# Kernel tuning notes

Hardware: AMD Instinct MI355X
Metric: run time of the kernel (lower is better)

The kernel has to match this reference:

```python
import jax, jax.numpy as jnp
import numpy as np

WINDOW_SIZE = 5  # hardcoded in module __init__


def local_window_mask(T, dtype=jnp.float32):
    # Faithful to torch code: start from triu(ones, diagonal=1) (value 1.0 for
    # j > i, NOT -inf!), then set entries outside the band |j - i| <= sz to -inf.
    sz = WINDOW_SIZE // 2
    i = jnp.arange(T)[:, None]
    j = jnp.arange(T)[None, :]
    upper = (j > i).astype(dtype)            # triu part contributes +1 bias
    in_band = jnp.abs(j - i) <= sz
    return jnp.where(in_band, upper, jnp.float32(-jnp.inf).astype(dtype))


def setup_inputs() -> dict:
    key = jax.random.key(0)
    kx, kq, kk, kv = jax.random.split(key, 4)
    B, T, C = 4, 4096, 64
    head_size = 64
    s = 1.0 / np.sqrt(C)
    return {
        "x": jax.random.normal(kx, (B, T, C), dtype=jnp.float32),
        "Wq": jax.random.normal(kq, (head_size, C), dtype=jnp.float32) * s,
        "Wk": jax.random.normal(kk, (head_size, C), dtype=jnp.float32) * s,
        "Wv": jax.random.normal(kv, (head_size, C), dtype=jnp.float32) * s,
    }


def reference(x, Wq, Wk, Wv):
    B, T, C = x.shape
    # nn.Linear(d_model, head_size, bias=False): y = x @ W.T
    q = jnp.einsum('btc,hc->bth', x, Wq)
    k = jnp.einsum('btc,hc->bth', x, Wk)
    v = jnp.einsum('btc,hc->bth', x, Wv)
    scale = jnp.asarray(C, x.dtype) ** -0.5   # scale uses input dim C
    scores = jnp.einsum('bth,bsh->bts', q, k) * scale + local_window_mask(T, x.dtype)
    attn = jax.nn.softmax(scores, axis=-1)    # original computes this twice; once suffices (same math)
    op = jnp.einsum('bts,bsh->bth', attn, v)
    return (op, attn)
```

## Files before the change

kernel.cpp:

```cpp
#include <hip/hip_runtime.h>

constexpr int B      = 4;
constexpr int T      = 4096;
constexpr int C      = 64;
constexpr int H      = 64;
constexpr int TILE   = 32;
constexpr int HALO   = 2;
constexpr int HR     = TILE + 2 * HALO;
constexpr int LS     = 68;
constexpr int NT     = 256;
constexpr int NTILES = T / TILE;

__device__ __forceinline__ void compute_mat(float (*__restrict__ dst)[LS],
                                            const float (*__restrict__ sXl)[LS],
                                            const float (*__restrict__ sWl)[LS],
                                            const int rows, const int srcOff,
                                            const int tid)
{
    const int nrt = rows >> 2;
    if (tid < nrt * 8) {
        const int rt = tid >> 3;
        const int h0 = (tid & 7) << 3;
        int r[4];
#pragma unroll
        for (int k = 0; k < 4; ++k) r[k] = rt + k * nrt + srcOff;

        float acc[4][8];
#pragma unroll
        for (int k = 0; k < 4; ++k)
#pragma unroll
            for (int j = 0; j < 8; ++j) acc[k][j] = 0.f;

        for (int c4 = 0; c4 < C; c4 += 4) {
            float xv[4][4];
#pragma unroll
            for (int k = 0; k < 4; ++k)
                *(float4*)&xv[k][0] = *(const float4*)&sXl[r[k]][c4];
#pragma unroll
            for (int cc = 0; cc < 4; ++cc) {
                const float4 wA = *(const float4*)&sWl[c4 + cc][h0];
                const float4 wB = *(const float4*)&sWl[c4 + cc][h0 + 4];
#pragma unroll
                for (int k = 0; k < 4; ++k) {
                    const float xs = xv[k][cc];
                    acc[k][0] = fmaf(xs, wA.x, acc[k][0]);
                    acc[k][1] = fmaf(xs, wA.y, acc[k][1]);
                    acc[k][2] = fmaf(xs, wA.z, acc[k][2]);
                    acc[k][3] = fmaf(xs, wA.w, acc[k][3]);
                    acc[k][4] = fmaf(xs, wB.x, acc[k][4]);
                    acc[k][5] = fmaf(xs, wB.y, acc[k][5]);
                    acc[k][6] = fmaf(xs, wB.z, acc[k][6]);
                    acc[k][7] = fmaf(xs, wB.w, acc[k][7]);
                }
            }
        }
#pragma unroll
        for (int k = 0; k < 4; ++k) {
            const int rr = r[k] - srcOff;
            *(float4*)&dst[rr][h0]     = make_float4(acc[k][0], acc[k][1], acc[k][2], acc[k][3]);
            *(float4*)&dst[rr][h0 + 4] = make_float4(acc[k][4], acc[k][5], acc[k][6], acc[k][7]);
        }
    }
}

__global__ __launch_bounds__(NT, 2)
void sparse_attn_fused(const float* __restrict__ x,
                       const float* __restrict__ Wq,
                       const float* __restrict__ Wk,
                       const float* __restrict__ Wv,
                       float* __restrict__ out)
{
    __shared__ float sX[HR][LS];
    __shared__ float sW[C][LS];
    __shared__ float sQ[TILE][LS];
    __shared__ float sK[HR][LS];
    __shared__ float sV[HR][LS];
    __shared__ float sS[TILE][8];

    const int tid  = threadIdx.x;
    const int b    = blockIdx.x / NTILES;
    const int tile = blockIdx.x % NTILES;
    const int row0 = tile * TILE;
    const float* xb = x + (size_t)b * T * C;
    const size_t attnBase = (size_t)B * T * H;
    float* attnBlock = out + attnBase + ((size_t)b * T + row0) * T;

    for (int s = tid; s < HR * (C / 4); s += NT) {
        const int lr = s >> 4;
        const int c4 = (s & 15) << 2;
        const int gr = row0 + lr - HALO;
        float4 v = make_float4(0.f, 0.f, 0.f, 0.f);
        if (gr >= 0 && gr < T) v = *(const float4*)(xb + (size_t)gr * C + c4);
        *(float4*)&sX[lr][c4] = v;
    }
    for (int s = tid; s < C * H; s += NT) sW[s & 63][s >> 6] = Wq[s];
    {
        float4* dst = (float4*)attnBlock;
        const float4 z = make_float4(0.f, 0.f, 0.f, 0.f);
        for (int s = tid; s < TILE * (T / 4); s += NT) dst[s] = z;
    }
    __syncthreads();

    compute_mat(sQ, sX, sW, TILE, HALO, tid);
    __syncthreads();

    for (int s = tid; s < C * H; s += NT) sW[s & 63][s >> 6] = Wk[s];
    __syncthreads();

    compute_mat(sK, sX, sW, HR, 0, tid);
    __syncthreads();

    if (tid < TILE * 5) {
        const int i  = tid / 5;
        const int dj = tid % 5;
        const int jg = row0 + i - HALO + dj;
        float sc = -__builtin_inff();
        if (jg >= 0 && jg < T) {
            float acc = 0.f;
#pragma unroll
            for (int h4 = 0; h4 < C; h4 += 4) {
                const float4 q = *(const float4*)&sQ[i][h4];
                const float4 k = *(const float4*)&sK[i + dj][h4];
                acc += q.x * k.x + q.y * k.y + q.z * k.z + q.w * k.w;
            }
            sc = acc * 0.125f + (dj > 2 ? 1.0f : 0.0f);
        }
        sS[i][dj] = sc;
    }
    for (int s = tid; s < C * H; s += NT) sW[s & 63][s >> 6] = Wv[s];
    __syncthreads();

    if (tid < TILE) {
        const int i  = tid;
        const int ig = row0 + i;
        float sc[5];
        float m = -__builtin_inff();
#pragma unroll
        for (int d = 0; d < 5; ++d) { sc[d] = sS[i][d]; m = fmaxf(m, sc[d]); }
        float p[5];
        float sum = 0.f;
#pragma unroll
        for (int d = 0; d < 5; ++d) { p[d] = expf(sc[d] - m); sum += p[d]; }
        const float inv = 1.f / sum;
        float* rowp = out + attnBase + ((size_t)b * T + ig) * T;
#pragma unroll
        for (int d = 0; d < 5; ++d) {
            const float pv = p[d] * inv;
            sS[i][d] = pv;
            const int j = ig - HALO + d;
            if (j >= 0 && j < T) rowp[j] = pv;
        }
    }
    __syncthreads();

    compute_mat(sV, sX, sW, HR, 0, tid);
    __syncthreads();

    for (int s = tid; s < TILE * H; s += NT) {
        const int h = s & 63;
        const int r = s >> 6;
        float acc = 0.f;
#pragma unroll
        for (int d = 0; d < 5; ++d) acc = fmaf(sS[r][d], sV[r + d][h], acc);
        out[((size_t)b * T + row0 + r) * H + h] = acc;
    }
}

extern "C" void kernel_launch(void* const* d_in, const int* in_sizes, int n_in,
                              void* d_out, int out_size, void* d_ws, size_t ws_size,
                              hipStream_t stream) {
    (void)in_sizes; (void)n_in; (void)d_ws; (void)ws_size; (void)out_size;
    const float* x  = (const float*)d_in[0];
    const float* Wq = (const float*)d_in[1];
    const float* Wk = (const float*)d_in[2];
    const float* Wv = (const float*)d_in[3];
    float* out = (float*)d_out;
    sparse_attn_fused<<<dim3(B * NTILES), dim3(NT), 0, stream>>>(x, Wq, Wk, Wv, out);
}
```

Measured before the change: 287.4 us.

## Split attention zero-fill into dedicated grid-stride blocks separate from compute blocks

The kernel now launches 2048 extra blocks that only zero-fill the off-band part of the attention matrix with a grid-stride float4 loop. The compute blocks no longer clear their own rows before doing the projections. They write the band region as whole float4 chunks with zeros padded in, so the two kinds of block never write the same address. The aim is to decouple the bandwidth-bound fill of the 256 MB matrix from the compute path so it spreads better across the GPU, at the cost of a per-element band check in the fill loop.

```diff
diff --git a/kernel.cpp b/kernel.cpp
--- a/kernel.cpp
+++ b/kernel.cpp
@@ -10,6 +10,10 @@
 constexpr int LS     = 68;
 constexpr int NT     = 256;
 constexpr int NTILES = T / TILE;
+constexpr int CBLOCKS = B * NTILES;
+constexpr int FBLOCKS = 2048;
+constexpr int T4     = T / 4;
+constexpr unsigned TOTAL4 = (unsigned)B * (unsigned)T * (unsigned)T4;
 
 __device__ __forceinline__ void compute_mat(float (*__restrict__ dst)[LS],
                                             const float (*__restrict__ sXl)[LS],
@@ -77,13 +81,27 @@
     __shared__ float sV[HR][LS];
     __shared__ float sS[TILE][8];
 
-    const int tid  = threadIdx.x;
+    const int tid = threadIdx.x;
+    const size_t attnBase = (size_t)B * T * H;
+
+    if (blockIdx.x >= CBLOCKS) {
+        float4* __restrict__ attn4 = (float4*)(out + attnBase);
+        const unsigned base   = (unsigned)(blockIdx.x - CBLOCKS) * NT + tid;
+        const unsigned stride = (unsigned)FBLOCKS * NT;
+        const float4 z = make_float4(0.f, 0.f, 0.f, 0.f);
+        for (unsigned n = base; n < TOTAL4; n += stride) {
+            const int c4 = (int)(n & (T4 - 1));
+            const int i  = (int)((n >> 10) & (T - 1));
+            const int j0 = c4 << 2;
+            if (j0 > i + HALO || j0 + 3 < i - HALO) attn4[n] = z;
+        }
+        return;
+    }
+
     const int b    = blockIdx.x / NTILES;
     const int tile = blockIdx.x % NTILES;
     const int row0 = tile * TILE;
     const float* xb = x + (size_t)b * T * C;
-    const size_t attnBase = (size_t)B * T * H;
-    float* attnBlock = out + attnBase + ((size_t)b * T + row0) * T;
 
     for (int s = tid; s < HR * (C / 4); s += NT) {
         const int lr = s >> 4;
@@ -94,11 +112,6 @@
         *(float4*)&sX[lr][c4] = v;
     }
     for (int s = tid; s < C * H; s += NT) sW[s & 63][s >> 6] = Wq[s];
-    {
-        float4* dst = (float4*)attnBlock;
-        const float4 z = make_float4(0.f, 0.f, 0.f, 0.f);
-        for (int s = tid; s < TILE * (T / 4); s += NT) dst[s] = z;
-    }
     __syncthreads();
 
     compute_mat(sQ, sX, sW, TILE, HALO, tid);
@@ -142,13 +155,20 @@
 #pragma unroll
         for (int d = 0; d < 5; ++d) { p[d] = expf(sc[d] - m); sum += p[d]; }
         const float inv = 1.f / sum;
+#pragma unroll
+        for (int d = 0; d < 5; ++d) sS[i][d] = p[d] * inv;
+
         float* rowp = out + attnBase + ((size_t)b * T + ig) * T;
+        const int cLo = (ig - HALO > 0 ? ig - HALO : 0) >> 2;
+        const int cHi = (ig + HALO < T - 1 ? ig + HALO : T - 1) >> 2;
+        for (int c = cLo; c <= cHi; ++c) {
+            float vv[4];
 #pragma unroll
-        for (int d = 0; d < 5; ++d) {
-            const float pv = p[d] * inv;
-            sS[i][d] = pv;
-            const int j = ig - HALO + d;
-            if (j >= 0 && j < T) rowp[j] = pv;
+            for (int q = 0; q < 4; ++q) {
+                const int d = (c << 2) + q - (ig - HALO);
+                vv[q] = (d >= 0 && d < 5) ? sS[i][d] : 0.f;
+            }
+            *(float4*)(rowp + (c << 2)) = make_float4(vv[0], vv[1], vv[2], vv[3]);
         }
     }
     __syncthreads();
@@ -175,5 +195,5 @@
     const float* Wk = (const float*)d_in[2];
     const float* Wv = (const float*)d_in[3];
     float* out = (float*)d_out;
-    sparse_attn_fused<<<dim3(B * NTILES), dim3(NT), 0, stream>>>(x, Wq, Wk, Wv, out);
+    sparse_attn_fused<<<dim3(CBLOCKS + FBLOCKS), dim3(NT), 0, stream>>>(x, Wq, Wk, Wv, out);
 }
```

After: 307.3 us. 1.07x slower.
